# Kernel tuning notes

Hardware: AMD Instinct MI355X
Metric: run time of the kernel (lower is better)

## Reference

```python
import jax, jax.numpy as jnp
from jax import lax
import numpy as np

DEPTH = 10  # matches init depth; n_nodes = 2**DEPTH - 1 = 1023


def setup_inputs() -> dict:
    key = jax.random.key(0)
    k1, k2, k3 = jax.random.split(key, 3)
    B, nIn, nOut = 65536, 1024, 1024
    n_nodes = 2 ** DEPTH - 1
    x = jax.random.normal(k1, (B, nIn), dtype=jnp.float32)
    # hyperspherical-shell init: unit-normalized gaussian rows
    w1s = jax.random.normal(k2, (n_nodes, nIn), dtype=jnp.float32)
    w1s = w1s / jnp.linalg.norm(w1s, axis=-1, keepdims=True)
    w2s = jax.random.normal(k3, (n_nodes, nOut), dtype=jnp.float32)
    w2s = w2s / jnp.linalg.norm(w2s, axis=-1, keepdims=True)
    return {"x": x, "w1s": w1s, "w2s": w2s}


def reference(x, w1s, w2s):
    B = x.shape[0]
    nOut = w2s.shape[1]

    def step(carry, _):
        node, y = carry                      # node: [B] int32, y: [B, nOut]
        lam = jnp.einsum('bi,bi->b', x, w1s[node])      # per-sample dot
        y = y + lam[:, None] * w2s[node]                 # accumulate scaled leaf vec
        node = node * 2 + 1 + (lam > 0).astype(node.dtype)  # descend tree
        return (node, y), None

    init = (jnp.zeros((B,), dtype=jnp.int32), jnp.zeros((B, nOut), dtype=x.dtype))
    (_, y), _ = lax.scan(step, init, None, length=DEPTH)
    return y
```

## Files before the change

kernel.cpp:

```cpp
#include <hip/hip_runtime.h>


#define FFF_DEPTH 10
#define N_IN 1024
#define N_OUT 1024
#define N_LEAF 512
#define LEAF_BASE 511
#define BIN_CAP 512
#define N_STAGE 31
#define ROUTE_THREADS 1024
#define ROUTE_BLOCKS 256
#define BLOCKS_PER_LEAF 8

typedef float f32x4 __attribute__((ext_vector_type(4)));

template<int CTRL, int ROW_MASK>
__device__ __forceinline__ float dpp_add(float v) {
    int sh = __builtin_amdgcn_update_dpp(0, __builtin_bit_cast(int, v),
                                         CTRL, ROW_MASK, 0xf, true);
    return v + __builtin_bit_cast(float, sh);
}

__device__ __forceinline__ float wave_sum(float p) {
    p = dpp_add<0x111, 0xf>(p);
    p = dpp_add<0x112, 0xf>(p);
    p = dpp_add<0x114, 0xf>(p);
    p = dpp_add<0x118, 0xf>(p);
    p = dpp_add<0x142, 0xa>(p);
    p = dpp_add<0x143, 0xc>(p);
    return __builtin_bit_cast(float,
        __builtin_amdgcn_readlane(__builtin_bit_cast(int, p), 63));
}

__device__ __forceinline__ void store_stream(f32x4 v, f32x4* addr) {
    asm volatile("global_store_dwordx4 %0, %1, off sc0 sc1 nt"
                 :: "v"(addr), "v"(v) : "memory");
}

#define ROUTE_LEVEL_BODY(dd, wa, wb)                                          \
    {                                                                         \
        f32x4 w0[4], w1v[4];                                                  \
        _Pragma("unroll")                                                     \
        for (int c = 0; c < 4; ++c) {                                         \
            w0[c] = (wa)[c * 64 + lane];                                      \
            w1v[c] = (wb)[c * 64 + lane];                                     \
        }                                                                     \
        float p0 = 0.f, p1 = 0.f, p2 = 0.f, p3 = 0.f;                         \
        float q0 = 0.f, q1 = 0.f, q2 = 0.f, q3 = 0.f;                         \
        _Pragma("unroll")                                                     \
        for (int c = 0; c < 4; ++c) {                                         \
            p0 += xv0[c][0] * w0[c][0];  q0 += xv1[c][0] * w1v[c][0];         \
            p1 += xv0[c][1] * w0[c][1];  q1 += xv1[c][1] * w1v[c][1];         \
            p2 += xv0[c][2] * w0[c][2];  q2 += xv1[c][2] * w1v[c][2];         \
            p3 += xv0[c][3] * w0[c][3];  q3 += xv1[c][3] * w1v[c][3];         \
        }                                                                     \
        const float lam0 = wave_sum((p0 + p1) + (p2 + p3));                   \
        const float lam1 = wave_sum((q0 + q1) + (q2 + q3));                   \
        const float pick = (lane < 16) ? lam0 : lam1;                         \
        myl = (sel == (dd)) ? pick : myl;                                     \
        n0 = n0 * 2 + 1 + (lam0 > 0.f ? 1 : 0);                               \
        n1 = n1 * 2 + 1 + (lam1 > 0.f ? 1 : 0);                               \
    }

__global__ __launch_bounds__(ROUTE_THREADS, 4) void route_kernel(
    const float* __restrict__ x,
    const float* __restrict__ w1s,
    float* __restrict__ lams16,
    int* __restrict__ bins,
    int* __restrict__ cnt,
    int B)
{
    extern __shared__ float w1_lds[];

    {
        f32x4* dst = reinterpret_cast<f32x4*>(w1_lds);
        const f32x4* src = reinterpret_cast<const f32x4*>(w1s);
        for (int i = threadIdx.x; i < N_STAGE * 256; i += ROUTE_THREADS)
            dst[i] = src[i];
    }
    __syncthreads();

    const int lane = threadIdx.x & 63;
    const int wslot = blockIdx.x * (ROUTE_THREADS / 64) + (threadIdx.x >> 6);
    const int wstride = gridDim.x * (ROUTE_THREADS / 64);
    const int npairs = B >> 1;
    const int sel = lane & 15;

    for (int pr = wslot; pr < npairs; pr += wstride) {
        const int b0 = pr * 2, b1 = b0 + 1;

        const f32x4* xa = reinterpret_cast<const f32x4*>(x + (size_t)b0 * N_IN);
        const f32x4* xb = reinterpret_cast<const f32x4*>(x + (size_t)b1 * N_IN);
        f32x4 xv0[4], xv1[4];
        #pragma unroll
        for (int c = 0; c < 4; ++c) {
            xv0[c] = __builtin_nontemporal_load(&xa[c * 64 + lane]);
            xv1[c] = __builtin_nontemporal_load(&xb[c * 64 + lane]);
        }

        float myl = 0.f;
        int n0 = 0, n1 = 0;

        #pragma unroll
        for (int d = 0; d < 5; ++d) {
            const f32x4* wa = reinterpret_cast<const f32x4*>(w1_lds + n0 * N_IN);
            const f32x4* wb = reinterpret_cast<const f32x4*>(w1_lds + n1 * N_IN);
            ROUTE_LEVEL_BODY(d, wa, wb)
        }
        #pragma unroll
        for (int d = 5; d < FFF_DEPTH; ++d) {
            const f32x4* wa = reinterpret_cast<const f32x4*>(w1s + (size_t)n0 * N_IN);
            const f32x4* wb = reinterpret_cast<const f32x4*>(w1s + (size_t)n1 * N_IN);
            ROUTE_LEVEL_BODY(d, wa, wb)
        }

        if (lane < 32) lams16[(size_t)b0 * 16 + lane] = (sel < FFF_DEPTH) ? myl : 0.f;

        if (lane == 0) {
            int l0 = ((n0 - 1) >> 1) - LEAF_BASE;
            int p = atomicAdd(&cnt[l0], 1);
            if (p < BIN_CAP) bins[l0 * BIN_CAP + p] = b0;
        }
        if (lane == 1) {
            int l1 = ((n1 - 1) >> 1) - LEAF_BASE;
            int p = atomicAdd(&cnt[l1], 1);
            if (p < BIN_CAP) bins[l1 * BIN_CAP + p] = b1;
        }
    }
}

__global__ void zero_cnt_kernel(int* __restrict__ cnt) {
    cnt[threadIdx.x] = 0;
}

__global__ __launch_bounds__(256, 4) void accum_kernel(
    const float* __restrict__ w2s,
    const float* __restrict__ lams16,
    const int* __restrict__ bins,
    const int* __restrict__ cnt,
    float* __restrict__ y)
{
    __shared__ float lds[FFF_DEPTH * N_OUT];
    const int leaf = blockIdx.x >> 3;
    const int part = blockIdx.x & 7;

    int nodes[FFF_DEPTH];
    int n = LEAF_BASE + leaf;
    #pragma unroll
    for (int d = FFF_DEPTH - 1; d >= 0; --d) { nodes[d] = n; n = (n - 1) >> 1; }

    const int tid = threadIdx.x;
    f32x4* lds4 = reinterpret_cast<f32x4*>(lds);
    #pragma unroll
    for (int d = 0; d < FFF_DEPTH; ++d) {
        const f32x4* src = reinterpret_cast<const f32x4*>(w2s + (size_t)nodes[d] * N_OUT);
        lds4[d * 256 + tid] = src[tid];
    }
    __syncthreads();

    int nsamp = cnt[leaf];
    if (nsamp > BIN_CAP) nsamp = BIN_CAP;
    const int nq = (nsamp + BLOCKS_PER_LEAF - 1) / BLOCKS_PER_LEAF;
    const int rs = part * nq;
    int re = rs + nq;
    if (re > nsamp) re = nsamp;

    const int lane = tid & 63, wv = tid >> 6;
    const int* mybin = bins + leaf * BIN_CAP;

    int p = rs + wv;

    for (; p + 4 < re; p += 8) {
        const int b0 = __builtin_amdgcn_readfirstlane(mybin[p]);
        const int b1 = __builtin_amdgcn_readfirstlane(mybin[p + 4]);
        const float lv0 = lams16[(size_t)b0 * 16 + (lane & 15)];
        const float lv1 = lams16[(size_t)b1 * 16 + (lane & 15)];

        f32x4 a0[4], a1[4];
        #pragma unroll
        for (int c = 0; c < 4; ++c) { a0[c] = (f32x4)0.f; a1[c] = (f32x4)0.f; }
        #pragma unroll
        for (int d = 0; d < FFF_DEPTH; ++d) {
            const float s0 = __builtin_bit_cast(float,
                __builtin_amdgcn_readlane(__builtin_bit_cast(int, lv0), d));
            const float s1 = __builtin_bit_cast(float,
                __builtin_amdgcn_readlane(__builtin_bit_cast(int, lv1), d));
            #pragma unroll
            for (int c = 0; c < 4; ++c) {
                const f32x4 w = lds4[d * 256 + c * 64 + lane];
                a0[c] += s0 * w;
                a1[c] += s1 * w;
            }
        }
        f32x4* y0 = reinterpret_cast<f32x4*>(y + (size_t)b0 * N_OUT);
        f32x4* y1 = reinterpret_cast<f32x4*>(y + (size_t)b1 * N_OUT);
        #pragma unroll
        for (int c = 0; c < 4; ++c) {
            store_stream(a0[c], &y0[c * 64 + lane]);
            store_stream(a1[c], &y1[c * 64 + lane]);
        }
    }

    for (; p < re; p += 4) {
        const int b = __builtin_amdgcn_readfirstlane(mybin[p]);
        const float lv = lams16[(size_t)b * 16 + (lane & 15)];
        f32x4 acc[4];
        #pragma unroll
        for (int c = 0; c < 4; ++c) acc[c] = (f32x4)0.f;
        #pragma unroll
        for (int d = 0; d < FFF_DEPTH; ++d) {
            const float s = __builtin_bit_cast(float,
                __builtin_amdgcn_readlane(__builtin_bit_cast(int, lv), d));
            #pragma unroll
            for (int c = 0; c < 4; ++c) acc[c] += s * lds4[d * 256 + c * 64 + lane];
        }
        f32x4* y4 = reinterpret_cast<f32x4*>(y + (size_t)b * N_OUT);
        #pragma unroll
        for (int c = 0; c < 4; ++c) store_stream(acc[c], &y4[c * 64 + lane]);
    }
}

__global__ __launch_bounds__(256, 4) void fff_mono_kernel(
    const float* __restrict__ x, const float* __restrict__ w1s,
    const float* __restrict__ w2s, float* __restrict__ y, int B)
{
    const int lane = threadIdx.x & 63;
    const int b = blockIdx.x * 4 + (threadIdx.x >> 6);
    if (b >= B) return;
    const f32x4* x4 = reinterpret_cast<const f32x4*>(x + (size_t)b * N_IN);
    f32x4 xv[4], acc[4];
    #pragma unroll
    for (int c = 0; c < 4; ++c) { xv[c] = __builtin_nontemporal_load(&x4[c*64+lane]); acc[c] = (f32x4)0.f; }
    int node = 0;
    #pragma unroll
    for (int d = 0; d < FFF_DEPTH; ++d) {
        const f32x4* w1 = reinterpret_cast<const f32x4*>(w1s + (size_t)node * N_IN);
        const f32x4* w2 = reinterpret_cast<const f32x4*>(w2s + (size_t)node * N_OUT);
        f32x4 w[4], v[4];
        #pragma unroll
        for (int c = 0; c < 4; ++c) { w[c] = w1[c*64+lane]; v[c] = w2[c*64+lane]; }
        float p0=0,p1=0,p2=0,p3=0;
        #pragma unroll
        for (int c = 0; c < 4; ++c) {
            p0 += xv[c][0]*w[c][0]; p1 += xv[c][1]*w[c][1];
            p2 += xv[c][2]*w[c][2]; p3 += xv[c][3]*w[c][3];
        }
        float lam = wave_sum((p0+p1)+(p2+p3));
        #pragma unroll
        for (int c = 0; c < 4; ++c) acc[c] += lam * v[c];
        node = node * 2 + 1 + (lam > 0.f ? 1 : 0);
    }
    f32x4* y4 = reinterpret_cast<f32x4*>(y + (size_t)b * N_OUT);
    #pragma unroll
    for (int c = 0; c < 4; ++c) store_stream(acc[c], &y4[c*64+lane]);
}

extern "C" void kernel_launch(void* const* d_in, const int* in_sizes, int n_in,
                              void* d_out, int out_size, void* d_ws, size_t ws_size,
                              hipStream_t stream) {
    const float* x   = (const float*)d_in[0];
    const float* w1s = (const float*)d_in[1];
    const float* w2s = (const float*)d_in[2];
    float* y = (float*)d_out;
    const int B = in_sizes[0] / N_IN;

    float* lams16 = (float*)d_ws;
    int*   bins   = (int*)(lams16 + (size_t)B * 16);
    int*   cnt    = bins + (size_t)N_LEAF * BIN_CAP;
    const size_t need = ((size_t)B * 16 + (size_t)N_LEAF * BIN_CAP + N_LEAF) * 4;

    if (ws_size < need) {
        fff_mono_kernel<<<(B + 3) / 4, 256, 0, stream>>>(x, w1s, w2s, y, B);
        return;
    }

    zero_cnt_kernel<<<1, N_LEAF, 0, stream>>>(cnt);
    route_kernel<<<ROUTE_BLOCKS, ROUTE_THREADS, N_STAGE * N_IN * sizeof(float), stream>>>(
        x, w1s, lams16, bins, cnt, B);
    accum_kernel<<<BLOCKS_PER_LEAF * N_LEAF, 256, 0, stream>>>(w2s, lams16, bins, cnt, y);
}
```

Measured before the change: 165.8 us.

## Speculatively compute both child dot products to overlap global loads with reductions

In the routing kernel, the global-memory levels now compute partial dot products for both children of the current node before the current node's wave reduction resolves. The correct child's partial is then selected, so the dependent load latency of each tree level is hidden behind the previous level's reduction. This doubles the global weight loads and FMAs on levels 5-9 and raises register pressure. The mono kernel is refactored to use a shared helper.

Result: slower. 208.8 us (+25.9%).

```diff
diff --git a/kernel.cpp b/kernel.cpp
--- a/kernel.cpp
+++ b/kernel.cpp
@@ -37,30 +37,19 @@
                  :: "v"(addr), "v"(v) : "memory");
 }
 
-#define ROUTE_LEVEL_BODY(dd, wa, wb)                                          \
-    {                                                                         \
-        f32x4 w0[4], w1v[4];                                                  \
-        _Pragma("unroll")                                                     \
-        for (int c = 0; c < 4; ++c) {                                         \
-            w0[c] = (wa)[c * 64 + lane];                                      \
-            w1v[c] = (wb)[c * 64 + lane];                                     \
-        }                                                                     \
-        float p0 = 0.f, p1 = 0.f, p2 = 0.f, p3 = 0.f;                         \
-        float q0 = 0.f, q1 = 0.f, q2 = 0.f, q3 = 0.f;                         \
-        _Pragma("unroll")                                                     \
-        for (int c = 0; c < 4; ++c) {                                         \
-            p0 += xv0[c][0] * w0[c][0];  q0 += xv1[c][0] * w1v[c][0];         \
-            p1 += xv0[c][1] * w0[c][1];  q1 += xv1[c][1] * w1v[c][1];         \
-            p2 += xv0[c][2] * w0[c][2];  q2 += xv1[c][2] * w1v[c][2];         \
-            p3 += xv0[c][3] * w0[c][3];  q3 += xv1[c][3] * w1v[c][3];         \
-        }                                                                     \
-        const float lam0 = wave_sum((p0 + p1) + (p2 + p3));                   \
-        const float lam1 = wave_sum((q0 + q1) + (q2 + q3));                   \
-        const float pick = (lane < 16) ? lam0 : lam1;                         \
-        myl = (sel == (dd)) ? pick : myl;                                     \
-        n0 = n0 * 2 + 1 + (lam0 > 0.f ? 1 : 0);                               \
-        n1 = n1 * 2 + 1 + (lam1 > 0.f ? 1 : 0);                               \
-    }
+__device__ __forceinline__ float row_partial(const f32x4* __restrict__ r,
+                                             const f32x4 xv[4], int lane) {
+    float p0 = 0.f, p1 = 0.f, p2 = 0.f, p3 = 0.f;
+    #pragma unroll
+    for (int c = 0; c < 4; ++c) {
+        const f32x4 w = r[c * 64 + lane];
+        p0 += xv[c][0] * w[0];
+        p1 += xv[c][1] * w[1];
+        p2 += xv[c][2] * w[2];
+        p3 += xv[c][3] * w[3];
+    }
+    return (p0 + p1) + (p2 + p3);
+}
 
 __global__ __launch_bounds__(ROUTE_THREADS, 4) void route_kernel(
     const float* __restrict__ x,
@@ -102,16 +91,62 @@
         int n0 = 0, n1 = 0;
 
         #pragma unroll
-        for (int d = 0; d < 5; ++d) {
-            const f32x4* wa = reinterpret_cast<const f32x4*>(w1_lds + n0 * N_IN);
-            const f32x4* wb = reinterpret_cast<const f32x4*>(w1_lds + n1 * N_IN);
-            ROUTE_LEVEL_BODY(d, wa, wb)
-        }
-        #pragma unroll
-        for (int d = 5; d < FFF_DEPTH; ++d) {
-            const f32x4* wa = reinterpret_cast<const f32x4*>(w1s + (size_t)n0 * N_IN);
-            const f32x4* wb = reinterpret_cast<const f32x4*>(w1s + (size_t)n1 * N_IN);
-            ROUTE_LEVEL_BODY(d, wa, wb)
+        for (int d = 0; d < 4; ++d) {
+            float pa = row_partial(reinterpret_cast<const f32x4*>(w1_lds + n0 * N_IN), xv0, lane);
+            float pb = row_partial(reinterpret_cast<const f32x4*>(w1_lds + n1 * N_IN), xv1, lane);
+            const float lamA = wave_sum(pa);
+            const float lamB = wave_sum(pb);
+            const float pick = (lane < 16) ? lamA : lamB;
+            myl = (sel == d) ? pick : myl;
+            n0 = n0 * 2 + 1 + (lamA > 0.f ? 1 : 0);
+            n1 = n1 * 2 + 1 + (lamB > 0.f ? 1 : 0);
+        }
+
+        float qa, qb;
+        {
+            float qaL = row_partial(reinterpret_cast<const f32x4*>(w1s + (size_t)(2 * n0 + 1) * N_IN), xv0, lane);
+            float qaR = row_partial(reinterpret_cast<const f32x4*>(w1s + (size_t)(2 * n0 + 2) * N_IN), xv0, lane);
+            float qbL = row_partial(reinterpret_cast<const f32x4*>(w1s + (size_t)(2 * n1 + 1) * N_IN), xv1, lane);
+            float qbR = row_partial(reinterpret_cast<const f32x4*>(w1s + (size_t)(2 * n1 + 2) * N_IN), xv1, lane);
+
+            float pa = row_partial(reinterpret_cast<const f32x4*>(w1_lds + n0 * N_IN), xv0, lane);
+            float pb = row_partial(reinterpret_cast<const f32x4*>(w1_lds + n1 * N_IN), xv1, lane);
+            const float lamA = wave_sum(pa);
+            const float lamB = wave_sum(pb);
+            const float pick = (lane < 16) ? lamA : lamB;
+            myl = (sel == 4) ? pick : myl;
+            const bool sA = lamA > 0.f, sB = lamB > 0.f;
+            n0 = n0 * 2 + 1 + (sA ? 1 : 0);
+            n1 = n1 * 2 + 1 + (sB ? 1 : 0);
+            qa = sA ? qaR : qaL;
+            qb = sB ? qbR : qbL;
+        }
+
+        #pragma unroll
+        for (int d = 5; d < 9; ++d) {
+            float caL = row_partial(reinterpret_cast<const f32x4*>(w1s + (size_t)(2 * n0 + 1) * N_IN), xv0, lane);
+            float caR = row_partial(reinterpret_cast<const f32x4*>(w1s + (size_t)(2 * n0 + 2) * N_IN), xv0, lane);
+            float cbL = row_partial(reinterpret_cast<const f32x4*>(w1s + (size_t)(2 * n1 + 1) * N_IN), xv1, lane);
+            float cbR = row_partial(reinterpret_cast<const f32x4*>(w1s + (size_t)(2 * n1 + 2) * N_IN), xv1, lane);
+
+            const float lamA = wave_sum(qa);
+            const float lamB = wave_sum(qb);
+            const float pick = (lane < 16) ? lamA : lamB;
+            myl = (sel == d) ? pick : myl;
+            const bool sA = lamA > 0.f, sB = lamB > 0.f;
+            n0 = n0 * 2 + 1 + (sA ? 1 : 0);
+            n1 = n1 * 2 + 1 + (sB ? 1 : 0);
+            qa = sA ? caR : caL;
+            qb = sB ? cbR : cbL;
+        }
+
+        {
+            const float lamA = wave_sum(qa);
+            const float lamB = wave_sum(qb);
+            const float pick = (lane < 16) ? lamA : lamB;
+            myl = (sel == 9) ? pick : myl;
+            n0 = n0 * 2 + 1 + (lamA > 0.f ? 1 : 0);
+            n1 = n1 * 2 + 1 + (lamB > 0.f ? 1 : 0);
         }
 
         if (lane < 32) lams16[(size_t)b0 * 16 + lane] = (sel < FFF_DEPTH) ? myl : 0.f;
@@ -236,18 +271,10 @@
     for (int d = 0; d < FFF_DEPTH; ++d) {
         const f32x4* w1 = reinterpret_cast<const f32x4*>(w1s + (size_t)node * N_IN);
         const f32x4* w2 = reinterpret_cast<const f32x4*>(w2s + (size_t)node * N_OUT);
-        f32x4 w[4], v[4];
-        #pragma unroll
-        for (int c = 0; c < 4; ++c) { w[c] = w1[c*64+lane]; v[c] = w2[c*64+lane]; }
-        float p0=0,p1=0,p2=0,p3=0;
-        #pragma unroll
-        for (int c = 0; c < 4; ++c) {
-            p0 += xv[c][0]*w[c][0]; p1 += xv[c][1]*w[c][1];
-            p2 += xv[c][2]*w[c][2]; p3 += xv[c][3]*w[c][3];
-        }
-        float lam = wave_sum((p0+p1)+(p2+p3));
-        #pragma unroll
-        for (int c = 0; c < 4; ++c) acc[c] += lam * v[c];
+        float p = row_partial(w1, xv, lane);
+        float lam = wave_sum(p);
+        #pragma unroll
+        for (int c = 0; c < 4; ++c) acc[c] += lam * w2[c*64+lane];
         node = node * 2 + 1 + (lam > 0.f ? 1 : 0);
     }
     f32x4* y4 = reinterpret_cast<f32x4*>(y + (size_t)b * N_OUT);
```
